# Kernel tuning notes

Hardware: AMD Instinct MI355X
Metric: run time of the kernel (lower is better)

## Reference

```python
import jax, jax.numpy as jnp
import numpy as np

TOKENS, D_MODEL, VOCAB = 8192, 1024, 32000


def setup_inputs() -> dict:
    key = jax.random.key(0)
    k1, k2, k3 = jax.random.split(key, 3)
    inp = jax.random.normal(k1, (TOKENS, D_MODEL), dtype=jnp.float32)
    proj_weight = jax.random.normal(k2, (VOCAB, D_MODEL), dtype=jnp.float32) * 0.02
    target = jax.random.randint(k3, (TOKENS,), 0, VOCAB, dtype=jnp.int64)
    return {"input": inp, "proj_weight": proj_weight, "target": target}


def reference(input, proj_weight, target):
    # Fused linear -> log_softmax -> NLL with reduction='sum'.
    # Original tiles over tokens/vocab with an online max/sum; the math is
    # exactly: loss = sum_t ( logsumexp_v(logits[t, :]) - logits[t, target[t]] )
    # with max/sum/target-score reductions done in float32 (fp_max/fp_sum/fp_target=True).
    logits = jnp.matmul(input, proj_weight.T).astype(jnp.float32)  # [tokens, vocab]
    lse = jax.nn.logsumexp(logits, axis=1)                          # [tokens]
    target_score = jnp.take_along_axis(logits, target[:, None].astype(jnp.int32), axis=1)[:, 0]
    return jnp.sum(lse - target_score)  # scalar, reduction='sum'
```

## Files before the change

### kernel.cpp

```cpp
#include <hip/hip_runtime.h>
#include <stdint.h>


#define TOKENS 8192
#define DMODEL 1024
#define VOCAB  32000

#define NBM8   (TOKENS / 128)
#define NBN8   (VOCAB / 128)
#define NWG8   (NBM8 * NBN8)

#define NBM    (TOKENS / 128)
#define NBN    (VOCAB / 128)
#define NWG    (NBM * NBN)
#define CHUNK  (NWG / 8)

typedef float  f32x4  __attribute__((ext_vector_type(4)));
typedef int    i32x8  __attribute__((ext_vector_type(8)));
typedef __bf16 bf16x8 __attribute__((ext_vector_type(8)));
typedef unsigned short u16;
typedef u16 u16x4 __attribute__((ext_vector_type(4)));

__device__ __forceinline__ u16 f2bf(float f) {
  union { float f; uint32_t u; } v; v.f = f;
  return (u16)((v.u + 0x7FFFu + ((v.u >> 16) & 1u)) >> 16);
}

__device__ __forceinline__ uint8_t f2e4m3(float x) {
  union { float f; uint32_t u; } v; v.f = x;
  const uint32_t s = (v.u >> 24) & 0x80u;
  const float ax = fabsf(x);
  if (ax >= 464.f) return (uint8_t)(s | 0x7E);
  if (ax < 0.015625f) {
    const int q = (int)rintf(ax * 512.f);
    return (uint8_t)(s | (uint32_t)q);
  }
  uint32_t u = v.u;
  u += 0x000FFFFFu + ((u >> 20) & 1u);
  const int E = (int)((u >> 23) & 0xFF) - 127;
  const uint32_t m3 = (u >> 20) & 0x7u;
  return (uint8_t)(s | (uint32_t)(((E + 7) << 3) | m3));
}

__device__ __forceinline__ void g2lds16(const void* gsrc, void* ldst) {
  __builtin_amdgcn_global_load_lds(
      (const __attribute__((address_space(1))) uint32_t*)(uintptr_t)gsrc,
      (__attribute__((address_space(3))) uint32_t*)(uintptr_t)ldst,
      16, 0, 0);
}

__global__ void convert_to_fp8(const float* __restrict__ in, uint8_t* __restrict__ out,
                               long long n, float scale) {
  long long i0 = ((long long)blockIdx.x * blockDim.x + threadIdx.x) * 8;
  long long stride = (long long)gridDim.x * blockDim.x * 8;
  for (long long base = i0; base < n; base += stride) {
    float4 a = *(const float4*)(in + base);
    float4 b = *(const float4*)(in + base + 4);
    uint8_t r[8] = { f2e4m3(a.x * scale), f2e4m3(a.y * scale),
                     f2e4m3(a.z * scale), f2e4m3(a.w * scale),
                     f2e4m3(b.x * scale), f2e4m3(b.y * scale),
                     f2e4m3(b.z * scale), f2e4m3(b.w * scale) };
    *(uint64_t*)(out + base) = *(const uint64_t*)r;
  }
}

__device__ __forceinline__ void stage_fp8(const uint8_t* __restrict__ G, uint8_t* L,
                                          int grow0, int k0, int wave, int lane) {
#pragma unroll
  for (int i = 0; i < 4; ++i) {
    const int c   = i * 4 + wave;
    const int row = c * 8 + (lane >> 3);
    const int col = ((lane & 7) * 16) ^ ((row & 7) << 4);
    g2lds16(G + (size_t)(grow0 + row) * DMODEL + k0 + col, (void*)(L + c * 1024));
  }
}

__device__ __forceinline__ void kstep_fp8(const uint8_t* As, const uint8_t* Bs,
                                          f32x4 acc[4][4],
                                          int wr, int wc, int l15, int l4) {
  const int swz = (l15 & 7) << 4;
  const int c0 = (l4 * 32) ^ swz;
  const int c1 = (l4 * 32 + 16) ^ swz;
  i32x8 a[4], b[4];
#pragma unroll
  for (int m = 0; m < 4; ++m) {
    const uint8_t* p = As + (wr * 64 + m * 16 + l15) * 128;
    *(uint4*)&a[m]       = *(const uint4*)(p + c0);
    *((uint4*)&a[m] + 1) = *(const uint4*)(p + c1);
  }
#pragma unroll
  for (int n = 0; n < 4; ++n) {
    const uint8_t* p = Bs + (wc * 64 + n * 16 + l15) * 128;
    *(uint4*)&b[n]       = *(const uint4*)(p + c0);
    *((uint4*)&b[n] + 1) = *(const uint4*)(p + c1);
  }
  __builtin_amdgcn_s_setprio(1);
#pragma unroll
  for (int m = 0; m < 4; ++m)
#pragma unroll
    for (int n = 0; n < 4; ++n)
      acc[m][n] = __builtin_amdgcn_mfma_scale_f32_16x16x128_f8f6f4(
          a[m], b[n], acc[m][n], 0, 0,
          0, 0x7F7F7F7F, 0, 0x7F7F7F7F);
  __builtin_amdgcn_s_setprio(0);
}

__global__ __launch_bounds__(256, 2)
void gemm_lse_fp8(const uint8_t* __restrict__ A8, const uint8_t* __restrict__ B8,
                  float* __restrict__ S) {
  __shared__ uint8_t smem[65536];
  uint8_t* A0 = smem;
  uint8_t* B0 = smem + 16384;
  uint8_t* A1 = smem + 32768;
  uint8_t* B1 = smem + 49152;

  const int tid  = threadIdx.x;
  const int lane = tid & 63;
  const int wave = tid >> 6;
  const int wr = wave >> 1, wc = wave & 1;
  const int l15 = lane & 15, l4 = lane >> 4;

  const int lid  = blockIdx.x;
  const int band = lid & 7;
  const int idx2 = lid >> 3;
  const int bn   = idx2 >> 3;
  const int bm   = band * 8 + (idx2 & 7);
  const int arow = bm * 128, brow = bn * 128;

  f32x4 acc[4][4];
#pragma unroll
  for (int m = 0; m < 4; ++m)
#pragma unroll
    for (int n = 0; n < 4; ++n) acc[m][n] = (f32x4)(0.f);

  stage_fp8(A8, A0, arow, 0, wave, lane);
  stage_fp8(B8, B0, brow, 0, wave, lane);

#pragma unroll 1
  for (int tt = 0; tt < 4; ++tt) {
    const int t0 = 2 * tt;
    __syncthreads();
    if (t0 + 1 < 8) {
      stage_fp8(A8, A1, arow, (t0 + 1) * 128, wave, lane);
      stage_fp8(B8, B1, brow, (t0 + 1) * 128, wave, lane);
    }
    kstep_fp8(A0, B0, acc, wr, wc, l15, l4);
    __syncthreads();
    if (t0 + 2 < 8) {
      stage_fp8(A8, A0, arow, (t0 + 2) * 128, wave, lane);
      stage_fp8(B8, B0, brow, (t0 + 2) * 128, wave, lane);
    }
    kstep_fp8(A1, B1, acc, wr, wc, l15, l4);
  }

#pragma unroll
  for (int m = 0; m < 4; ++m) {
#pragma unroll
    for (int j = 0; j < 4; ++j) {
      float v = 0.f;
#pragma unroll
      for (int n = 0; n < 4; ++n) v += __expf(acc[m][n][j] * 0.0625f);
      v += __shfl_xor(v, 1);
      v += __shfl_xor(v, 2);
      v += __shfl_xor(v, 4);
      v += __shfl_xor(v, 8);
      if (l15 == 0) {
        const int row = arow + wr * 64 + m * 16 + l4 * 4 + j;
        atomicAdd(&S[row], v);
      }
    }
  }
}

__global__ __launch_bounds__(256)
void gemm_lse_fb(const float* __restrict__ Af, const float* __restrict__ Bf,
                 float* __restrict__ S) {
  __shared__ u16 As[128 * 64];
  __shared__ u16 Bs[128 * 64];

  const int tid  = threadIdx.x;
  const int lane = tid & 63;
  const int wave = tid >> 6;
  const int wr = wave >> 1, wc = wave & 1;
  const int l15 = lane & 15, l4 = lane >> 4;

  const int lid = blockIdx.x;
  const int wid = (lid & 7) * CHUNK + (lid >> 3);
  const int bm = wid & (NBM - 1);
  const int bn = wid / NBM;

  f32x4 acc[4][4];
#pragma unroll
  for (int m = 0; m < 4; ++m)
#pragma unroll
    for (int n = 0; n < 4; ++n) acc[m][n] = (f32x4)(0.f);

  for (int kt = 0; kt < DMODEL / 64; ++kt) {
    const int k0 = kt * 64;
    {
      const int row = tid >> 4;
      const int kq  = (tid & 15) * 4;
#pragma unroll
      for (int r = 0; r < 8; ++r) {
        const int rr = r * 16 + row;
        const int kd = kq ^ ((rr & 7) << 3);
        float4 a4 = *(const float4*)(Af + (size_t)(bm * 128 + rr) * DMODEL + k0 + kq);
        float4 b4 = *(const float4*)(Bf + (size_t)(bn * 128 + rr) * DMODEL + k0 + kq);
        u16x4 ap = { f2bf(a4.x), f2bf(a4.y), f2bf(a4.z), f2bf(a4.w) };
        u16x4 bp = { f2bf(b4.x), f2bf(b4.y), f2bf(b4.z), f2bf(b4.w) };
        *(u16x4*)&As[rr * 64 + kd] = ap;
        *(u16x4*)&Bs[rr * 64 + kd] = bp;
      }
    }
    __syncthreads();
#pragma unroll
    for (int kk = 0; kk < 2; ++kk) {
      bf16x8 av[4], bv[4];
      const int swz = (l15 & 7) << 3;
      const int kc  = (kk * 32 + l4 * 8) ^ swz;
#pragma unroll
      for (int m = 0; m < 4; ++m)
        av[m] = *(const bf16x8*)&As[(wr * 64 + m * 16 + l15) * 64 + kc];
#pragma unroll
      for (int n = 0; n < 4; ++n)
        bv[n] = *(const bf16x8*)&Bs[(wc * 64 + n * 16 + l15) * 64 + kc];
#pragma unroll
      for (int m = 0; m < 4; ++m)
#pragma unroll
        for (int n = 0; n < 4; ++n)
          acc[m][n] = __builtin_amdgcn_mfma_f32_16x16x32_bf16(av[m], bv[n], acc[m][n], 0, 0, 0);
    }
    __syncthreads();
  }

#pragma unroll
  for (int m = 0; m < 4; ++m) {
#pragma unroll
    for (int j = 0; j < 4; ++j) {
      float v = 0.f;
#pragma unroll
      for (int n = 0; n < 4; ++n) v += __expf(acc[m][n][j]);
      v += __shfl_xor(v, 1);
      v += __shfl_xor(v, 2);
      v += __shfl_xor(v, 4);
      v += __shfl_xor(v, 8);
      if (l15 == 0) {
        const int row = bm * 128 + wr * 64 + m * 16 + l4 * 4 + j;
        atomicAdd(&S[row], v);
      }
    }
  }
}

__global__ void target_score_k(const float* __restrict__ inp, const float* __restrict__ W,
                               const int* __restrict__ tgt, float* __restrict__ ts) {
  const int gtid = blockIdx.x * blockDim.x + threadIdx.x;
  const int t = gtid >> 6;
  const int lane = threadIdx.x & 63;
  if (t >= TOKENS) return;
  bool allhi0 = true, anylo = false;
  for (int i = 0; i < 64; ++i) {
    if (tgt[2 * i + 1] != 0) allhi0 = false;
    if (tgt[2 * i] != 0) anylo = true;
  }
  const int v = (allhi0 && anylo) ? tgt[2 * t] : tgt[t];
  const float4* xr = (const float4*)(inp + (size_t)t * DMODEL);
  const float4* wr = (const float4*)(W + (size_t)v * DMODEL);
  float s = 0.f;
#pragma unroll
  for (int i = 0; i < 4; ++i) {
    float4 a = xr[lane + 64 * i];
    float4 b = wr[lane + 64 * i];
    s += a.x * b.x + a.y * b.y + a.z * b.z + a.w * b.w;
  }
#pragma unroll
  for (int off = 32; off >= 1; off >>= 1) s += __shfl_xor(s, off);
  if (lane == 0) ts[t] = s;
}

__global__ void finalize_k(const float* __restrict__ S, const float* __restrict__ ts,
                           float* __restrict__ out) {
  __shared__ float red[16];
  float s = 0.f;
  for (int t = threadIdx.x; t < TOKENS; t += blockDim.x) s += __logf(S[t]) - ts[t];
#pragma unroll
  for (int off = 32; off >= 1; off >>= 1) s += __shfl_xor(s, off);
  const int wave = threadIdx.x >> 6, lane = threadIdx.x & 63;
  if (lane == 0) red[wave] = s;
  __syncthreads();
  if (threadIdx.x == 0) {
    float tot = 0.f;
    for (int w = 0; w < (int)(blockDim.x >> 6); ++w) tot += red[w];
    out[0] = tot;
  }
}

extern "C" void kernel_launch(void* const* d_in, const int* in_sizes, int n_in,
                              void* d_out, int out_size, void* d_ws, size_t ws_size,
                              hipStream_t stream) {
  const float* inp = (const float*)d_in[0];
  const float* W   = (const float*)d_in[1];
  const int*   tgt = (const int*)d_in[2];
  float* out = (float*)d_out;

  char* ws = (char*)d_ws;
  float* S  = (float*)ws;
  float* ts = (float*)(ws + 32 * 1024);
  const size_t offA = 64 * 1024;
  const size_t offB = offA + (size_t)TOKENS * DMODEL;
  const size_t need = offB + (size_t)VOCAB * DMODEL;
  const bool preconv = ws_size >= need;

  hipMemsetAsync(S, 0, TOKENS * sizeof(float), stream);

  if (preconv) {
    uint8_t* A8 = (uint8_t*)(ws + offA);
    uint8_t* B8 = (uint8_t*)(ws + offB);
    convert_to_fp8<<<4096, 256, 0, stream>>>(inp, A8, (long long)TOKENS * DMODEL, 1.0f);
    convert_to_fp8<<<4096, 256, 0, stream>>>(W, B8, (long long)VOCAB * DMODEL, 16.0f);
    gemm_lse_fp8<<<NWG8, 256, 0, stream>>>(A8, B8, S);
  } else {
    gemm_lse_fb<<<NWG, 256, 0, stream>>>(inp, W, S);
  }
  target_score_k<<<(TOKENS * 64) / 256, 256, 0, stream>>>(inp, W, tgt, ts);
  finalize_k<<<1, 1024, 0, stream>>>(S, ts, out);
}
```

Measured before the change: 429.3 us.

## Pre-tile FP8 operands into MFMA fragment layout and use 32x32x64 MFMA

The FP8 conversion kernels now write A and B in a tiled layout matching the MFMA register fragments, so the GEMM stages contiguous 1 KB chunks into LDS and reads fragments linearly without swizzling. The GEMM switches from 16x16x128 to 32x32x64 scaled MFMA, and the block tile grows from 128x128 to 128x256. K steps shrink from 128 to 64, which doubles the number of iterations. The intent is to cut LDS read overhead and raise MFMA efficiency, at the cost of more accumulator registers and a gather-style read in the conversion.

```diff
diff --git a/kernel.cpp b/kernel.cpp
--- a/kernel.cpp
+++ b/kernel.cpp
@@ -6,18 +6,19 @@
 #define DMODEL 1024
 #define VOCAB  32000
 
-#define NBM8   (TOKENS / 128)
-#define NBN8   (VOCAB / 128)
-#define NWG8   (NBM8 * NBN8)
+#define NBM32  (TOKENS / 128)
+#define NBN32  (VOCAB / 256)
+#define NWG32  (NBM32 * NBN32)
 
 #define NBM    (TOKENS / 128)
 #define NBN    (VOCAB / 128)
 #define NWG    (NBM * NBN)
 #define CHUNK  (NWG / 8)
 
-typedef float  f32x4  __attribute__((ext_vector_type(4)));
-typedef int    i32x8  __attribute__((ext_vector_type(8)));
-typedef __bf16 bf16x8 __attribute__((ext_vector_type(8)));
+typedef float  f32x4   __attribute__((ext_vector_type(4)));
+typedef float  f32x16  __attribute__((ext_vector_type(16)));
+typedef int    i32x8   __attribute__((ext_vector_type(8)));
+typedef __bf16 bf16x8  __attribute__((ext_vector_type(8)));
 typedef unsigned short u16;
 typedef u16 u16x4 __attribute__((ext_vector_type(4)));
 
@@ -49,123 +50,132 @@
       16, 0, 0);
 }
 
-__global__ void convert_to_fp8(const float* __restrict__ in, uint8_t* __restrict__ out,
-                               long long n, float scale) {
-  long long i0 = ((long long)blockIdx.x * blockDim.x + threadIdx.x) * 8;
-  long long stride = (long long)gridDim.x * blockDim.x * 8;
-  for (long long base = i0; base < n; base += stride) {
-    float4 a = *(const float4*)(in + base);
-    float4 b = *(const float4*)(in + base + 4);
-    uint8_t r[8] = { f2e4m3(a.x * scale), f2e4m3(a.y * scale),
-                     f2e4m3(a.z * scale), f2e4m3(a.w * scale),
-                     f2e4m3(b.x * scale), f2e4m3(b.y * scale),
-                     f2e4m3(b.z * scale), f2e4m3(b.w * scale) };
-    *(uint64_t*)(out + base) = *(const uint64_t*)r;
-  }
-}
-
-__device__ __forceinline__ void stage_fp8(const uint8_t* __restrict__ G, uint8_t* L,
-                                          int grow0, int k0, int wave, int lane) {
-#pragma unroll
-  for (int i = 0; i < 4; ++i) {
-    const int c   = i * 4 + wave;
-    const int row = c * 8 + (lane >> 3);
-    const int col = ((lane & 7) * 16) ^ ((row & 7) << 4);
-    g2lds16(G + (size_t)(grow0 + row) * DMODEL + k0 + col, (void*)(L + c * 1024));
-  }
-}
-
-__device__ __forceinline__ void kstep_fp8(const uint8_t* As, const uint8_t* Bs,
-                                          f32x4 acc[4][4],
-                                          int wr, int wc, int l15, int l4) {
-  const int swz = (l15 & 7) << 4;
-  const int c0 = (l4 * 32) ^ swz;
-  const int c1 = (l4 * 32 + 16) ^ swz;
-  i32x8 a[4], b[4];
-#pragma unroll
-  for (int m = 0; m < 4; ++m) {
-    const uint8_t* p = As + (wr * 64 + m * 16 + l15) * 128;
-    *(uint4*)&a[m]       = *(const uint4*)(p + c0);
-    *((uint4*)&a[m] + 1) = *(const uint4*)(p + c1);
-  }
-#pragma unroll
-  for (int n = 0; n < 4; ++n) {
-    const uint8_t* p = Bs + (wc * 64 + n * 16 + l15) * 128;
-    *(uint4*)&b[n]       = *(const uint4*)(p + c0);
-    *((uint4*)&b[n] + 1) = *(const uint4*)(p + c1);
+__global__ void convert_fp8_tiled(const float* __restrict__ in, uint8_t* __restrict__ out,
+                                  long long total, int NR, int log2ts, float scale) {
+  const long long step = (long long)gridDim.x * blockDim.x * 8;
+  for (long long d = ((long long)blockIdx.x * blockDim.x + threadIdx.x) * 8;
+       d < total; d += step) {
+    const long long tile = d >> log2ts;
+    const int x  = (int)(d & ((1 << log2ts) - 1));
+    const int sub = x >> 11;
+    const int l   = (x >> 5) & 63;
+    const int b0  = x & 31;
+    const int rb  = (int)(tile >> 4);
+    const int kt  = (int)(tile & 15);
+    const int row = rb * NR + sub * 32 + (l & 31);
+    const int k   = kt * 64 + (l >> 5) * 32 + b0;
+    const float* src = in + (size_t)row * DMODEL + k;
+    const float4 f0 = *(const float4*)src;
+    const float4 f1 = *(const float4*)(src + 4);
+    uint8_t r[8] = { f2e4m3(f0.x * scale), f2e4m3(f0.y * scale),
+                     f2e4m3(f0.z * scale), f2e4m3(f0.w * scale),
+                     f2e4m3(f1.x * scale), f2e4m3(f1.y * scale),
+                     f2e4m3(f1.z * scale), f2e4m3(f1.w * scale) };
+    *(uint64_t*)(out + d) = *(const uint64_t*)r;
+  }
+}
+
+template <int NCHUNK>
+__device__ __forceinline__ void stage_lin(const uint8_t* __restrict__ src, uint8_t* dst,
+                                          int wave, int lane) {
+#pragma unroll
+  for (int p = 0; p < NCHUNK / 4; ++p) {
+    const int c = p * 4 + wave;
+    g2lds16(src + c * 1024 + lane * 16, (void*)(dst + c * 1024));
+  }
+}
+
+__device__ __forceinline__ void kstep32(const uint8_t* As, const uint8_t* Bs,
+                                        f32x16 (&acc)[2][4],
+                                        int wr, int wc, int lane) {
+  i32x8 a[2], b[4];
+  const uint8_t* ap = As + (wr * 2) * 2048 + lane * 32;
+#pragma unroll
+  for (int mi = 0; mi < 2; ++mi) {
+    *(uint4*)&a[mi]       = *(const uint4*)(ap + mi * 2048);
+    *((uint4*)&a[mi] + 1) = *(const uint4*)(ap + mi * 2048 + 16);
+  }
+  const uint8_t* bp = Bs + (wc * 4) * 2048 + lane * 32;
+#pragma unroll
+  for (int ni = 0; ni < 4; ++ni) {
+    *(uint4*)&b[ni]       = *(const uint4*)(bp + ni * 2048);
+    *((uint4*)&b[ni] + 1) = *(const uint4*)(bp + ni * 2048 + 16);
   }
   __builtin_amdgcn_s_setprio(1);
 #pragma unroll
-  for (int m = 0; m < 4; ++m)
-#pragma unroll
-    for (int n = 0; n < 4; ++n)
-      acc[m][n] = __builtin_amdgcn_mfma_scale_f32_16x16x128_f8f6f4(
-          a[m], b[n], acc[m][n], 0, 0,
+  for (int mi = 0; mi < 2; ++mi)
+#pragma unroll
+    for (int ni = 0; ni < 4; ++ni)
+      acc[mi][ni] = __builtin_amdgcn_mfma_scale_f32_32x32x64_f8f6f4(
+          a[mi], b[ni], acc[mi][ni], 0, 0,
           0, 0x7F7F7F7F, 0, 0x7F7F7F7F);
   __builtin_amdgcn_s_setprio(0);
 }
 
 __global__ __launch_bounds__(256, 2)
-void gemm_lse_fp8(const uint8_t* __restrict__ A8, const uint8_t* __restrict__ B8,
-                  float* __restrict__ S) {
-  __shared__ uint8_t smem[65536];
+void gemm_lse_fp8v2(const uint8_t* __restrict__ A8, const uint8_t* __restrict__ B8,
+                    float* __restrict__ S) {
+  __shared__ uint8_t smem[49152];
   uint8_t* A0 = smem;
-  uint8_t* B0 = smem + 16384;
-  uint8_t* A1 = smem + 32768;
-  uint8_t* B1 = smem + 49152;
+  uint8_t* B0 = smem + 8192;
+  uint8_t* A1 = smem + 24576;
+  uint8_t* B1 = smem + 32768;
 
   const int tid  = threadIdx.x;
   const int lane = tid & 63;
   const int wave = tid >> 6;
   const int wr = wave >> 1, wc = wave & 1;
-  const int l15 = lane & 15, l4 = lane >> 4;
 
   const int lid  = blockIdx.x;
   const int band = lid & 7;
   const int idx2 = lid >> 3;
   const int bn   = idx2 >> 3;
   const int bm   = band * 8 + (idx2 & 7);
-  const int arow = bm * 128, brow = bn * 128;
-
-  f32x4 acc[4][4];
-#pragma unroll
-  for (int m = 0; m < 4; ++m)
-#pragma unroll
-    for (int n = 0; n < 4; ++n) acc[m][n] = (f32x4)(0.f);
-
-  stage_fp8(A8, A0, arow, 0, wave, lane);
-  stage_fp8(B8, B0, brow, 0, wave, lane);
+  const int arow = bm * 128;
+
+  const uint8_t* Abase = A8 + (size_t)(bm * 16) * 8192;
+  const uint8_t* Bbase = B8 + (size_t)(bn * 16) * 16384;
+
+  f32x16 acc[2][4];
+#pragma unroll
+  for (int mi = 0; mi < 2; ++mi)
+#pragma unroll
+    for (int ni = 0; ni < 4; ++ni) acc[mi][ni] = (f32x16)(0.f);
+
+  stage_lin<8>(Abase, A0, wave, lane);
+  stage_lin<16>(Bbase, B0, wave, lane);
 
 #pragma unroll 1
-  for (int tt = 0; tt < 4; ++tt) {
+  for (int tt = 0; tt < 8; ++tt) {
     const int t0 = 2 * tt;
     __syncthreads();
-    if (t0 + 1 < 8) {
-      stage_fp8(A8, A1, arow, (t0 + 1) * 128, wave, lane);
-      stage_fp8(B8, B1, brow, (t0 + 1) * 128, wave, lane);
-    }
-    kstep_fp8(A0, B0, acc, wr, wc, l15, l4);
+    if (t0 + 1 < 16) {
+      stage_lin<8>(Abase + (size_t)(t0 + 1) * 8192, A1, wave, lane);
+      stage_lin<16>(Bbase + (size_t)(t0 + 1) * 16384, B1, wave, lane);
+    }
+    kstep32(A0, B0, acc, wr, wc, lane);
     __syncthreads();
-    if (t0 + 2 < 8) {
-      stage_fp8(A8, A0, arow, (t0 + 2) * 128, wave, lane);
-      stage_fp8(B8, B0, brow, (t0 + 2) * 128, wave, lane);
-    }
-    kstep_fp8(A1, B1, acc, wr, wc, l15, l4);
-  }
-
-#pragma unroll
-  for (int m = 0; m < 4; ++m) {
-#pragma unroll
-    for (int j = 0; j < 4; ++j) {
+    if (t0 + 2 < 16) {
+      stage_lin<8>(Abase + (size_t)(t0 + 2) * 8192, A0, wave, lane);
+      stage_lin<16>(Bbase + (size_t)(t0 + 2) * 16384, B0, wave, lane);
+    }
+    kstep32(A1, B1, acc, wr, wc, lane);
+  }
+
+#pragma unroll
+  for (int mi = 0; mi < 2; ++mi) {
+#pragma unroll
+    for (int r = 0; r < 16; ++r) {
       float v = 0.f;
 #pragma unroll
-      for (int n = 0; n < 4; ++n) v += __expf(acc[m][n][j] * 0.0625f);
+      for (int ni = 0; ni < 4; ++ni) v += __expf(acc[mi][ni][r] * 0.0625f);
       v += __shfl_xor(v, 1);
       v += __shfl_xor(v, 2);
       v += __shfl_xor(v, 4);
       v += __shfl_xor(v, 8);
-      if (l15 == 0) {
-        const int row = arow + wr * 64 + m * 16 + l4 * 4 + j;
+      v += __shfl_xor(v, 16);
+      if ((lane & 31) == 0) {
+        const int row = arow + (wr * 2 + mi) * 32 + (r & 3) + 8 * (r >> 2) + 4 * (lane >> 5);
         atomicAdd(&S[row], v);
       }
     }
@@ -307,8 +317,10 @@
   float* S  = (float*)ws;
   float* ts = (float*)(ws + 32 * 1024);
   const size_t offA = 64 * 1024;
-  const size_t offB = offA + (size_t)TOKENS * DMODEL;
-  const size_t need = offB + (size_t)VOCAB * DMODEL;
+  const long long totalA = (long long)TOKENS * DMODEL;
+  const long long totalB = (long long)VOCAB * DMODEL;
+  const size_t offB = offA + (size_t)totalA;
+  const size_t need = offB + (size_t)totalB;
   const bool preconv = ws_size >= need;
 
   hipMemsetAsync(S, 0, TOKENS * sizeof(float), stream);
@@ -316,9 +328,9 @@
   if (preconv) {
     uint8_t* A8 = (uint8_t*)(ws + offA);
     uint8_t* B8 = (uint8_t*)(ws + offB);
-    convert_to_fp8<<<4096, 256, 0, stream>>>(inp, A8, (long long)TOKENS * DMODEL, 1.0f);
-    convert_to_fp8<<<4096, 256, 0, stream>>>(W, B8, (long long)VOCAB * DMODEL, 16.0f);
-    gemm_lse_fp8<<<NWG8, 256, 0, stream>>>(A8, B8, S);
+    convert_fp8_tiled<<<4096, 256, 0, stream>>>(inp, A8, totalA, 128, 13, 1.0f);
+    convert_fp8_tiled<<<16000, 256, 0, stream>>>(W, B8, totalB, 256, 14, 16.0f);
+    gemm_lse_fp8v2<<<NWG32, 256, 0, stream>>>(A8, B8, S);
   } else {
     gemm_lse_fb<<<NWG, 256, 0, stream>>>(inp, W, S);
   }
```

Measured after the change: 376.2 us. 1.14x faster.
